# Kernel tuning notes

Measured on AMD Instinct MI355X. Metric: run time of the kernel, lower is better.

The kernel has to match this reference:

```python
import jax, jax.numpy as jnp
import numpy as np

B, N, C, H, R = 8, 1024, 768, 12, 64
HD = C // H


def setup_inputs() -> dict:
    key = jax.random.key(0)
    ks = jax.random.split(key, 16)
    def nrm(k, shape, s=0.02):
        return jax.random.normal(k, shape, jnp.float32) * s
    return {
        'x': jax.random.normal(ks[0], (B, N, C), jnp.float32),
        'Wqkv': nrm(ks[1], (3 * C, C)),
        'ssf_scale1': 1.0 + nrm(ks[2], (3 * C,)),
        'ssf_shift1': nrm(ks[3], (3 * C,)),
        'Wa': nrm(ks[4], (R, C)),            # LoRA down (sliced to sample_LoRA_dim)
        'Wb': nrm(ks[5], (3 * C, R)),        # LoRA up
        'Wrouter': nrm(ks[6], (2 * H * 3, C)),
        'brouter': nrm(ks[7], (2 * H * 3,)),
        'Wad_down': nrm(ks[8], (R, C)),      # parallel adapter down
        'bad_down': nrm(ks[9], (R,)),
        'Wad_up': nrm(ks[10], (3 * C, R)),   # parallel adapter up -> 3*dim
        'bad_up': nrm(ks[11], (3 * C,)),
        'Wproj': nrm(ks[12], (C, C)),
        'bproj': nrm(ks[13], (C,)),
        'ssf_scale2': 1.0 + nrm(ks[14], (C,)),
        'ssf_shift2': nrm(ks[15], (C,)),
    }


def reference(x, Wqkv, ssf_scale1, ssf_shift1, Wa, Wb, Wrouter, brouter,
              Wad_down, bad_down, Wad_up, bad_up, Wproj, bproj,
              ssf_scale2, ssf_shift2):
    Bx, Nx, Cx = x.shape
    scale = (Cx // H) ** -0.5

    def split_qkv(t):
        t = t.reshape(Bx, Nx, 3, H, Cx // H).transpose(2, 0, 3, 1, 4)
        return t[0], t[1], t[2]

    # base QKV with SSF scale-shift
    q, k, v = split_qkv((x @ Wqkv.T) * ssf_scale1 + ssf_shift1)
    # LoRA delta (dropout inactive at eval)
    ql, kl, vl = split_qkv((x @ Wa.T) @ Wb.T)
    # parallel adapter delta
    qp, kp, vp = split_qkv(jax.nn.gelu(x @ Wad_down.T + bad_down, approximate=False) @ Wad_up.T + bad_up)
    # router gating: sigmoid logits -> [B,N,3,H,2]
    rs = jax.nn.sigmoid(x @ Wrouter.T + brouter).reshape(Bx, Nx, 3, H, 2)
    # faithful to source: raw reshape [B,N,3,H] -> [B,N,H,3] (index-mixing), then transpose(1,2)
    rl = rs[..., 0].reshape(Bx, Nx, H, 3).transpose(0, 2, 1, 3)  # [B,H,N,3]
    rp = rs[..., 1].reshape(Bx, Nx, H, 3).transpose(0, 2, 1, 3)
    q = q + ql * rl[..., 0:1]
    k = k + kl * rl[..., 1:2] + kp * rp[..., 1:2]
    v = v + vl * rl[..., 2:3] + vp * rp[..., 2:3]
    # standard attention (prefix path disabled: prefix_dim=0)
    attn = jax.nn.softmax(jnp.einsum('bhnd,bhmd->bhnm', q, k) * scale, axis=-1)
    o = jnp.einsum('bhnm,bhmd->bhnd', attn, v).transpose(0, 2, 1, 3).reshape(Bx, Nx, Cx)
    return (o @ Wproj.T + bproj) * ssf_scale2 + ssf_shift2
```

## Files before the change

### kernel.cpp

```cpp
#include <hip/hip_runtime.h>
#include <math.h>

typedef unsigned short u16;
typedef unsigned int u32;
typedef short s16x8 __attribute__((ext_vector_type(8)));
typedef float f32x4 __attribute__((ext_vector_type(4)));
typedef float f32x16 __attribute__((ext_vector_type(16)));
typedef u16 u16x4 __attribute__((ext_vector_type(4)));

#define DEVI __device__ __forceinline__

DEVI u16 f2bf(float f) {
  unsigned u = __builtin_bit_cast(unsigned, f);
  u += 0x7fffu + ((u >> 16) & 1u);
  return (u16)(u >> 16);
}

DEVI u32 pkbf_hu(float a, float b) {
  const u32 ua = __builtin_bit_cast(u32, a) + 0x8000u;
  const u32 ub = __builtin_bit_cast(u32, b) + 0x8000u;
  return __builtin_amdgcn_perm(ub, ua, 0x07060302u);
}

DEVI f32x4 zero4() { f32x4 z; z[0]=0.f; z[1]=0.f; z[2]=0.f; z[3]=0.f; return z; }

DEVI float xor32_max(float x) { return fmaxf(x, __shfl_xor(x, 32, 64)); }
DEVI float xor32_sum(float x) { return x + __shfl_xor(x, 32, 64); }

#define MFMA16(a,b,c) __builtin_amdgcn_mfma_f32_16x16x32_bf16((a),(b),(c),0,0,0)
#define MFMA32(a,b,c) __builtin_amdgcn_mfma_f32_32x32x16_bf16((a),(b),(c),0,0,0)

#define GLD16(gp, lp) __builtin_amdgcn_global_load_lds( \
  (const __attribute__((address_space(1))) void*)(const void*)(gp), \
  (__attribute__((address_space(3))) void*)(void*)(lp), 16, 0, 0)

#define WAITVM(N) asm volatile("s_waitcnt vmcnt(" #N ")" ::: "memory")
#define WAITLG0() asm volatile("s_waitcnt lgkmcnt(0)" ::: "memory")
#define SBAR() __builtin_amdgcn_s_barrier()


__global__ __launch_bounds__(256) void prep_x(const float* __restrict__ x,
                                              u16* __restrict__ Aaug) {
  const int i = blockIdx.x * 256 + threadIdx.x;
  if (i >= 8192 * 192) return;
  const int row = i / 192, c4 = (i - row * 192) * 4;
  const float4 v = *(const float4*)(x + (size_t)row * 768 + c4);
  u16x4 o; o[0]=f2bf(v.x); o[1]=f2bf(v.y); o[2]=f2bf(v.z); o[3]=f2bf(v.w);
  *(u16x4*)(Aaug + (size_t)row * 896 + c4) = o;
}

__global__ __launch_bounds__(256) void prep_w(
    const float* __restrict__ Wqkv, const float* __restrict__ s1,
    const float* __restrict__ Wb, const float* __restrict__ Wup,
    const float* __restrict__ Wa, const float* __restrict__ Wdn,
    const float* __restrict__ Wr, const float* __restrict__ Wp,
    u16* __restrict__ Baug, u16* __restrict__ Wsm, u16* __restrict__ Wpj) {
  const int i = blockIdx.x * 256 + threadIdx.x;
  const int N1 = 2304 * 896, N2 = N1 + 256 * 768, N3 = N2 + 768 * 768;
  if (i < N1) {
    const int c = i / 896, kk = i - c * 896;
    float v;
    if (kk < 768)      v = Wqkv[(size_t)c * 768 + kk] * s1[c];
    else if (kk < 832) v = Wb[(size_t)c * 64 + (kk - 768)];
    else               v = Wup[(size_t)c * 64 + (kk - 832)];
    Baug[i] = f2bf(v);
  } else if (i < N2) {
    const int j = i - N1; const int r = j / 768, kk = j - r * 768;
    float v = 0.0f;
    if (r < 64)       v = Wa[(size_t)r * 768 + kk];
    else if (r < 128) v = Wdn[(size_t)(r - 64) * 768 + kk];
    else if (r < 200) v = Wr[(size_t)(r - 128) * 768 + kk];
    Wsm[j] = f2bf(v);
  } else if (i < N3) {
    const int j = i - N2;
    Wpj[j] = f2bf(Wp[j]);
  }
}


template <int MODE>
__global__ __launch_bounds__(256)
void gemm_mfma(const u16* __restrict__ A, int lda,
               const u16* __restrict__ Bt, int ldb,
               const float* __restrict__ p0, const float* __restrict__ p1,
               const float* __restrict__ p2,
               u16* __restrict__ ob0, u16* __restrict__ ob1, u16* __restrict__ ob2,
               float* __restrict__ of0,
               const float* __restrict__ gates) {
  __shared__ __align__(16) u16 lds[3][8192];
  __shared__ float glds[2][2][128];
  const int tid = threadIdx.x;
  const int w = tid >> 6, l = tid & 63;
  const int rl = l & 15, gq = l >> 4;
  const int wrow = (w >> 1) * 64, wcol = (w & 1) * 64;
  const int br = blockIdx.x, bc = blockIdx.y;
  const int nt = (MODE == 2) ? 28 : 24;

  const int srow = l >> 2;
  const int sslot = (l & 3) ^ ((srow >> 1) & 3);
  const u16* aSrc = A + (size_t)(br * 128 + w * 32 + srow) * lda + sslot * 8;
  const u16* bSrc = Bt + (size_t)(bc * 128 + w * 32 + srow) * ldb + sslot * 8;

  int tq = 0;
  if constexpr (MODE == 2) {
    const int g = bc * 2 + (w & 1);
    tq = g / 12;
  }

  auto kt_of = [&](int t) {
    if constexpr (MODE == 2) return (t < 2) ? 26 + t : ((t < 4) ? 22 + t : t - 4);
    else return t;
  };
  auto stage = [&](int kt, int buf) {
    const size_t k0 = (size_t)kt * 32;
    GLD16(aSrc + k0, &lds[buf][(w * 32) * 32]);
    GLD16(aSrc + k0 + (size_t)16 * lda, &lds[buf][(w * 32 + 16) * 32]);
    GLD16(bSrc + k0, &lds[buf][4096 + (w * 32) * 32]);
    GLD16(bSrc + k0 + (size_t)16 * ldb, &lds[buf][4096 + (w * 32 + 16) * 32]);
  };

  stage(kt_of(0), 0);
  stage(kt_of(1), 1);
  if constexpr (MODE == 2) {
    const int gsel = tid >> 7, rr = tid & 127;
    const int gg = bc * 2 + gsel;
    const int tt = gg / 12, hh = gg % 12;
    const int f = hh * 3 + tt;
    const int ridx = (f / 12) * 24 + (f % 12) * 2;
    glds[gsel][0][rr] = gates[(size_t)(br * 128 + rr) * 72 + ridx];
    glds[gsel][1][rr] = gates[(size_t)(br * 128 + rr) * 72 + ridx + 1];
    WAITLG0();
  }

  f32x4 acc[4][4];
#pragma unroll
  for (int i = 0; i < 4; ++i)
#pragma unroll
    for (int j = 0; j < 4; ++j) acc[i][j] = zero4();

  for (int t = 0; t < nt; ++t) {
    const int buf = t % 3;
    if (t + 2 < nt) stage(kt_of(t + 2), (t + 2) % 3);
    if (t < nt - 2)       WAITVM(8);
    else if (t == nt - 2) WAITVM(4);
    else                  WAITVM(0);
    SBAR();

    const int sl = gq ^ ((rl >> 1) & 3);
    s16x8 af[4], bfv[4];
#pragma unroll
    for (int fr = 0; fr < 4; ++fr) {
      const int row = wrow + fr * 16 + rl;
      af[fr] = *(const s16x8*)&lds[buf][row * 32 + sl * 8];
    }
#pragma unroll
    for (int fc = 0; fc < 4; ++fc) {
      const int row = wcol + fc * 16 + rl;
      bfv[fc] = *(const s16x8*)&lds[buf][4096 + row * 32 + sl * 8];
    }
#pragma unroll
    for (int fr = 0; fr < 4; ++fr)
#pragma unroll
      for (int fc = 0; fc < 4; ++fc)
        acc[fr][fc] = MFMA16(af[fr], bfv[fc], acc[fr][fc]);

    if constexpr (MODE == 2) {
      if (t == 1 || t == 3) {
        const int wsel = w & 1;
        const bool ad = (t == 1);
#pragma unroll
        for (int fr = 0; fr < 4; ++fr)
#pragma unroll
          for (int r = 0; r < 4; ++r) {
            const int rloc = wrow + fr * 16 + gq * 4 + r;
            const float gl = glds[wsel][0][rloc];
            float s;
            if (ad) { const float gp = glds[wsel][1][rloc]; s = (tq > 0) ? gp / gl : 0.0f; }
            else s = gl;
#pragma unroll
            for (int fc = 0; fc < 4; ++fc) acc[fr][fc][r] *= s;
          }
      }
    }
    SBAR();
  }

  if constexpr (MODE == 0) {
#pragma unroll
    for (int fc = 0; fc < 4; ++fc) {
      const int col = bc * 128 + wcol + fc * 16 + rl;
#pragma unroll
      for (int fr = 0; fr < 4; ++fr)
#pragma unroll
        for (int r = 0; r < 4; ++r) {
          const int grow = br * 128 + wrow + fr * 16 + gq * 4 + r;
          const float v = acc[fr][fc][r];
          if (col < 64) {
            ob0[(size_t)grow * 896 + 768 + col] = f2bf(v);
          } else if (col < 128) {
            const float u = v + p0[col - 64];
            const float gv = 0.5f * u * (1.0f + erff(u * 0.70710678118654752f));
            ob0[(size_t)grow * 896 + 832 + (col - 64)] = f2bf(gv);
          } else if (col < 200) {
            const float z = v + p1[col - 128];
            of0[(size_t)grow * 72 + (col - 128)] = 1.0f / (1.0f + expf(-z));
          }
        }
    }
  } else if constexpr (MODE == 1) {
#pragma unroll
    for (int fc = 0; fc < 4; ++fc) {
      const int col = bc * 128 + wcol + fc * 16 + rl;
      const float bb = p0[col], sc = p1[col], sf = p2[col];
#pragma unroll
      for (int fr = 0; fr < 4; ++fr)
#pragma unroll
        for (int r = 0; r < 4; ++r) {
          const int grow = br * 128 + wrow + fr * 16 + gq * 4 + r;
          of0[(size_t)grow * 768 + col] = (acc[fr][fc][r] + bb) * sc + sf;
        }
    }
  } else {
    const int wsel = w & 1;
    const int bq = br >> 3;
    const int n0 = (br & 7) * 128;
    const int cbase = bc * 128 + wcol;
    const int hh = (cbase % 768) / 64;
    float s1v[4], buv[4];
#pragma unroll
    for (int fc = 0; fc < 4; ++fc) {
      const int col = cbase + fc * 16 + rl;
      s1v[fc] = p0[col];
      buv[fc] = (tq > 0) ? p1[col] : 0.0f;
    }
    if (tq < 2) {
      u16* L = (u16*)&lds[0][0] + (size_t)w * 4096;
      u16* dst = (tq == 0) ? ob0 : ob1;
      const float osc = (tq == 0) ? 0.125f : 1.0f;
#pragma unroll
      for (int fr = 0; fr < 4; ++fr)
#pragma unroll
        for (int r = 0; r < 4; ++r) {
          const int nloc = fr * 16 + gq * 4 + r;
          const float gp = glds[wsel][1][wrow + nloc];
#pragma unroll
          for (int fc = 0; fc < 4; ++fc) {
            const int d = fc * 16 + rl;
            const float v = (acc[fr][fc][r] + s1v[fc] + gp * buv[fc]) * osc;
            L[nloc * 64 + (d ^ (gq << 4))] = f2bf(v);
          }
        }
      const size_t rowbase = (size_t)(bq * 12 + hh) * 1024 + n0 + wrow;
#pragma unroll
      for (int it = 0; it < 8; ++it) {
        const int nloc = it * 8 + (l >> 3);
        const int sl8 = l & 7;
        const s16x8 val =
            *(const s16x8*)&L[nloc * 64 + ((sl8 * 8) ^ (((nloc >> 2) & 3) << 4))];
        *(s16x8*)(dst + (rowbase + nloc) * 64 + sl8 * 8) = val;
      }
    } else {
      u16* L = (u16*)&lds[0][0] + (size_t)w * 4096;
#pragma unroll
      for (int fr = 0; fr < 4; ++fr)
#pragma unroll
        for (int r = 0; r < 4; ++r) {
          const int rloc = wrow + fr * 16 + gq * 4 + r;
          const float gp = glds[wsel][1][rloc];
          const int nloc = fr * 16 + gq * 4 + r;
#pragma unroll
          for (int fc = 0; fc < 4; ++fc) {
            const int d = fc * 16 + rl;
            const float v = acc[fr][fc][r] + s1v[fc] + gp * buv[fc];
            L[(d * 64 + nloc) ^ ((d & 7) << 3)] = f2bf(v);
          }
        }
      const int nw = n0 + wrow;
#pragma unroll
      for (int it = 0; it < 8; ++it) {
        const int d = it * 8 + (l >> 3);
        const int slot = l & 7;
        const s16x8 val = *(const s16x8*)&L[d * 64 + ((slot ^ (d & 7)) << 3)];
        *(s16x8*)(ob2 + ((size_t)(bq * 12 + hh) * 64 + d) * 1024 + nw + slot * 8) = val;
      }
    }
  }
}


__global__ __launch_bounds__(256)
void attn2_kernel(const u16* __restrict__ Q, const u16* __restrict__ K,
                  const u16* __restrict__ VT, u16* __restrict__ AO) {
  __shared__ __align__(16) u16 kv[3][8192];
  const int tid = threadIdx.x, w = tid >> 6, l = tid & 63;
  const int l31 = l & 31, hi = l >> 5;
  const int bh = blockIdx.x % 96, qt = blockIdx.x / 96;
  const size_t kb = (size_t)bh * (1024 * 64);
  const float LOG2E = 1.4426950408889634f;
  const float THR = 5.545177f;

  const int q0 = qt * 128 + w * 32;
  s16x8 qf[4];
  {
    const u16* qp = Q + kb + (size_t)(q0 + l31) * 64 + hi * 8;
#pragma unroll
    for (int ks = 0; ks < 4; ++ks) qf[ks] = *(const s16x8*)(qp + ks * 16);
  }

  const int srow = l >> 3;
  const int sslot = (l & 7) ^ srow;
  const u16* kSrc = K + kb + (size_t)(w * 16 + srow) * 64 + sslot * 8;
  const u16* vSrc = VT + kb + (size_t)(w * 16 + srow) * 1024 + sslot * 8;
  auto stage = [&](int t, int buf) {
    const int kv0 = t * 64;
    GLD16(kSrc + (size_t)kv0 * 64, &kv[buf][(w * 16) * 64]);
    GLD16(kSrc + (size_t)kv0 * 64 + 8 * 64, &kv[buf][(w * 16 + 8) * 64]);
    GLD16(vSrc + kv0, &kv[buf][4096 + (w * 16) * 64]);
    GLD16(vSrc + kv0 + 8 * 1024, &kv[buf][4096 + (w * 16 + 8) * 64]);
  };

  f32x16 o0, o1;
#pragma unroll
  for (int r = 0; r < 16; ++r) { o0[r] = 0.f; o1[r] = 0.f; }
  float m = -1.0e30f, lsum = 0.f;

  const int swz = l31 & 7;

  stage(0, 0);
  stage(1, 1);

  for (int t = 0; t < 16; ++t) {
    const int buf = t % 3;
    if (t + 2 < 16) stage(t + 2, (t + 2) % 3);
    if (t < 14)       WAITVM(8);
    else if (t == 14) WAITVM(4);
    else              WAITVM(0);
    SBAR();

    f32x16 sA, sB;
#pragma unroll
    for (int r = 0; r < 16; ++r) { sA[r] = 0.f; sB[r] = 0.f; }
#pragma unroll
    for (int ks = 0; ks < 4; ++ks) {
      const int slot = (ks * 2 + hi) ^ swz;
      const s16x8 k0 = *(const s16x8*)&kv[buf][l31 * 64 + slot * 8];
      const s16x8 k1 = *(const s16x8*)&kv[buf][(32 + l31) * 64 + slot * 8];
      sA = MFMA32(k0, qf[ks], sA);
      sB = MFMA32(k1, qf[ks], sB);
    }

    float pm = sA[0];
#pragma unroll
    for (int r = 1; r < 16; ++r) pm = fmaxf(pm, sA[r]);
#pragma unroll
    for (int r = 0; r < 16; ++r) pm = fmaxf(pm, sB[r]);
    pm = xor32_max(pm);

    const bool need = pm > m + THR;
    if (__any(need)) {
      const float mnew = need ? pm : m;
      const float corr = __builtin_amdgcn_exp2f((m - mnew) * LOG2E);
      m = mnew;
      lsum *= corr;
#pragma unroll
      for (int r = 0; r < 16; ++r) {
        const int qrow = (r & 3) + 8 * (r >> 2) + 4 * hi;
        const float cr = __shfl(corr, qrow, 64);
        o0[r] *= cr; o1[r] *= cr;
      }
    }

    const float mL = m * LOG2E;
    float ps = 0.f;
#pragma unroll
    for (int r = 0; r < 16; ++r) {
      const float p = __builtin_amdgcn_exp2f(__builtin_fmaf(sA[r], LOG2E, -mL));
      sA[r] = p; ps += p;
    }
#pragma unroll
    for (int r = 0; r < 16; ++r) {
      const float p = __builtin_amdgcn_exp2f(__builtin_fmaf(sB[r], LOG2E, -mL));
      sB[r] = p; ps += p;
    }
    lsum += xor32_sum(ps);

    s16x8 pf[4];
#pragma unroll
    for (int s = 0; s < 4; ++s) {
      const f32x16 P = (s < 2) ? sA : sB;
      const int b = 8 * (s & 1);
      const u32 A0 = pkbf_hu(P[b + 0], P[b + 1]);
      const u32 A1 = pkbf_hu(P[b + 2], P[b + 3]);
      const u32 A2 = pkbf_hu(P[b + 4], P[b + 5]);
      const u32 A3 = pkbf_hu(P[b + 6], P[b + 7]);
      const u32 B0 = (u32)__shfl_xor((int)A0, 32, 64);
      const u32 B1 = (u32)__shfl_xor((int)A1, 32, 64);
      const u32 B2 = (u32)__shfl_xor((int)A2, 32, 64);
      const u32 B3 = (u32)__shfl_xor((int)A3, 32, 64);
      union { u32 u[4]; s16x8 v; } pk;
      pk.u[0] = hi ? B2 : A0;
      pk.u[1] = hi ? B3 : A1;
      pk.u[2] = hi ? A2 : B0;
      pk.u[3] = hi ? A3 : B1;
      pf[s] = pk.v;
    }

#pragma unroll
    for (int s = 0; s < 4; ++s) {
      const int slot = (s * 2 + hi) ^ swz;
      const s16x8 v0 = *(const s16x8*)&kv[buf][4096 + l31 * 64 + slot * 8];
      const s16x8 v1 = *(const s16x8*)&kv[buf][4096 + (32 + l31) * 64 + slot * 8];
      o0 = MFMA32(pf[s], v0, o0);
      o1 = MFMA32(pf[s], v1, o1);
    }
    SBAR();
  }

  const float invl = 1.0f / lsum;
  const int bq = bh / 12, h = bh % 12;
#pragma unroll
  for (int r = 0; r < 16; ++r) {
    const int qrow = (r & 3) + 8 * (r >> 2) + 4 * hi;
    const float ir = __shfl(invl, qrow, 64);
    const int n = q0 + qrow;
    u16* dst = AO + ((size_t)bq * 1024 + n) * 768 + h * 64 + l31;
    dst[0]  = f2bf(o0[r] * ir);
    dst[32] = f2bf(o1[r] * ir);
  }
}


extern "C" void kernel_launch(void* const* d_in, const int* in_sizes, int n_in,
                              void* d_out, int out_size, void* d_ws, size_t ws_size,
                              hipStream_t stream) {
  (void)in_sizes; (void)n_in; (void)out_size; (void)ws_size;
  const float* x    = (const float*)d_in[0];
  const float* Wqkv = (const float*)d_in[1];
  const float* s1   = (const float*)d_in[2];
  const float* sh1  = (const float*)d_in[3];
  const float* Wa   = (const float*)d_in[4];
  const float* Wb   = (const float*)d_in[5];
  const float* Wr   = (const float*)d_in[6];
  const float* brt  = (const float*)d_in[7];
  const float* Wdn  = (const float*)d_in[8];
  const float* bdn  = (const float*)d_in[9];
  const float* Wup  = (const float*)d_in[10];
  const float* bup  = (const float*)d_in[11];
  const float* Wp   = (const float*)d_in[12];
  const float* bpj  = (const float*)d_in[13];
  const float* sc2  = (const float*)d_in[14];
  const float* sf2  = (const float*)d_in[15];
  float* out = (float*)d_out;

  char* ws = (char*)d_ws;
  size_t off = 0;
  auto take = [&](size_t bytes) -> void* {
    void* p = ws + off;
    off = (off + bytes + 255) & ~(size_t)255;
    return p;
  };
  u16* Aaug = (u16*)take(8192UL * 896 * 2);
  u16* Baug = (u16*)take(2304UL * 896 * 2);
  u16* Wsm  = (u16*)take(256UL * 768 * 2);
  u16* Wpj  = (u16*)take(768UL * 768 * 2);
  float* gates = (float*)take(8192UL * 72 * 4);
  u16* qb  = (u16*)take(96UL * 1024 * 64 * 2);
  u16* kbf = (u16*)take(96UL * 1024 * 64 * 2);
  u16* vtb = (u16*)take(96UL * 64 * 1024 * 2);
  u16* ao  = (u16*)take(8192UL * 768 * 2);

  prep_x<<<dim3(6144), dim3(256), 0, stream>>>(x, Aaug);
  prep_w<<<dim3(11136), dim3(256), 0, stream>>>(Wqkv, s1, Wb, Wup, Wa, Wdn, Wr, Wp,
                                                Baug, Wsm, Wpj);
  gemm_mfma<0><<<dim3(64, 2), dim3(256), 0, stream>>>(
      Aaug, 896, Wsm, 768, bdn, brt, nullptr, Aaug, nullptr, nullptr, gates, nullptr);
  gemm_mfma<2><<<dim3(64, 18), dim3(256), 0, stream>>>(
      Aaug, 896, Baug, 896, sh1, bup, nullptr, qb, kbf, vtb, nullptr, gates);
  attn2_kernel<<<dim3(768), dim3(256), 0, stream>>>(qb, kbf, vtb, ao);
  gemm_mfma<1><<<dim3(64, 6), dim3(256), 0, stream>>>(
      ao, 768, Wpj, 768, bpj, sc2, sf2, nullptr, nullptr, nullptr, out, nullptr);
}
```

Baseline: 174.2 us.

## Enlarge QKV GEMM tile to 256 rows with 512-thread blocks

The main QKV GEMM (MODE 2) now uses 256x128 tiles computed by 8 waves instead of 128x128 by 4 waves, which halves the grid along M. Each wave now stages one B row chunk instead of two, so each B tile is loaded once for twice as many A rows and global/LDS traffic for B drops. The vmcnt waits, gate LDS buffer and epilogue row indexing are adjusted to match. In exchange LDS use per block grows, the grid has fewer blocks (576), and the epilogue, which reuses lds per wave, has to remain correct with 8 waves.

Measured after the change: 179.8 us. 3.2% more time.

```diff
diff --git a/kernel.cpp b/kernel.cpp
--- a/kernel.cpp
+++ b/kernel.cpp
@@ -79,7 +79,7 @@
 
 
 template <int MODE>
-__global__ __launch_bounds__(256)
+__global__ __launch_bounds__((MODE == 2) ? 512 : 256)
 void gemm_mfma(const u16* __restrict__ A, int lda,
                const u16* __restrict__ Bt, int ldb,
                const float* __restrict__ p0, const float* __restrict__ p1,
@@ -87,19 +87,24 @@
                u16* __restrict__ ob0, u16* __restrict__ ob1, u16* __restrict__ ob2,
                float* __restrict__ of0,
                const float* __restrict__ gates) {
-  __shared__ __align__(16) u16 lds[3][8192];
-  __shared__ float glds[2][2][128];
+  constexpr int BM   = (MODE == 2) ? 256 : 128;
+  constexpr int BUFU = (MODE == 2) ? 12288 : 8192;
+  constexpr int BOFF = (MODE == 2) ? 8192 : 4096;
+  constexpr int nt   = (MODE == 2) ? 28 : 24;
+
+  __shared__ __align__(16) u16 lds[3][BUFU];
+  __shared__ float glds[2][2][BM];
   const int tid = threadIdx.x;
   const int w = tid >> 6, l = tid & 63;
   const int rl = l & 15, gq = l >> 4;
   const int wrow = (w >> 1) * 64, wcol = (w & 1) * 64;
   const int br = blockIdx.x, bc = blockIdx.y;
-  const int nt = (MODE == 2) ? 28 : 24;
 
   const int srow = l >> 2;
   const int sslot = (l & 3) ^ ((srow >> 1) & 3);
-  const u16* aSrc = A + (size_t)(br * 128 + w * 32 + srow) * lda + sslot * 8;
-  const u16* bSrc = Bt + (size_t)(bc * 128 + w * 32 + srow) * ldb + sslot * 8;
+  const u16* aSrc = A + (size_t)(br * BM + w * 32 + srow) * lda + sslot * 8;
+  const int bwrow = (MODE == 2) ? w * 16 : w * 32;
+  const u16* bSrc = Bt + (size_t)(bc * 128 + bwrow + srow) * ldb + sslot * 8;
 
   int tq = 0;
   if constexpr (MODE == 2) {
@@ -115,20 +120,24 @@
     const size_t k0 = (size_t)kt * 32;
     GLD16(aSrc + k0, &lds[buf][(w * 32) * 32]);
     GLD16(aSrc + k0 + (size_t)16 * lda, &lds[buf][(w * 32 + 16) * 32]);
-    GLD16(bSrc + k0, &lds[buf][4096 + (w * 32) * 32]);
-    GLD16(bSrc + k0 + (size_t)16 * ldb, &lds[buf][4096 + (w * 32 + 16) * 32]);
+    if constexpr (MODE == 2) {
+      GLD16(bSrc + k0, &lds[buf][BOFF + (w * 16) * 32]);
+    } else {
+      GLD16(bSrc + k0, &lds[buf][BOFF + (w * 32) * 32]);
+      GLD16(bSrc + k0 + (size_t)16 * ldb, &lds[buf][BOFF + (w * 32 + 16) * 32]);
+    }
   };
 
   stage(kt_of(0), 0);
   stage(kt_of(1), 1);
   if constexpr (MODE == 2) {
-    const int gsel = tid >> 7, rr = tid & 127;
+    const int gsel = tid >> 8, rr = tid & 255;
     const int gg = bc * 2 + gsel;
     const int tt = gg / 12, hh = gg % 12;
     const int f = hh * 3 + tt;
     const int ridx = (f / 12) * 24 + (f % 12) * 2;
-    glds[gsel][0][rr] = gates[(size_t)(br * 128 + rr) * 72 + ridx];
-    glds[gsel][1][rr] = gates[(size_t)(br * 128 + rr) * 72 + ridx + 1];
+    glds[gsel][0][rr] = gates[(size_t)(br * BM + rr) * 72 + ridx];
+    glds[gsel][1][rr] = gates[(size_t)(br * BM + rr) * 72 + ridx + 1];
     WAITLG0();
   }
 
@@ -141,9 +150,15 @@
   for (int t = 0; t < nt; ++t) {
     const int buf = t % 3;
     if (t + 2 < nt) stage(kt_of(t + 2), (t + 2) % 3);
-    if (t < nt - 2)       WAITVM(8);
-    else if (t == nt - 2) WAITVM(4);
-    else                  WAITVM(0);
+    if constexpr (MODE == 2) {
+      if (t < nt - 2)       WAITVM(6);
+      else if (t == nt - 2) WAITVM(3);
+      else                  WAITVM(0);
+    } else {
+      if (t < nt - 2)       WAITVM(8);
+      else if (t == nt - 2) WAITVM(4);
+      else                  WAITVM(0);
+    }
     SBAR();
 
     const int sl = gq ^ ((rl >> 1) & 3);
@@ -156,7 +171,7 @@
 #pragma unroll
     for (int fc = 0; fc < 4; ++fc) {
       const int row = wcol + fc * 16 + rl;
-      bfv[fc] = *(const s16x8*)&lds[buf][4096 + row * 32 + sl * 8];
+      bfv[fc] = *(const s16x8*)&lds[buf][BOFF + row * 32 + sl * 8];
     }
 #pragma unroll
     for (int fr = 0; fr < 4; ++fr)
@@ -222,8 +237,8 @@
     }
   } else {
     const int wsel = w & 1;
-    const int bq = br >> 3;
-    const int n0 = (br & 7) * 128;
+    const int bq = br >> 2;
+    const int n0 = (br & 3) * 256;
     const int cbase = bc * 128 + wcol;
     const int hh = (cbase % 768) / 64;
     float s1v[4], buv[4];
@@ -474,7 +489,7 @@
                                                 Baug, Wsm, Wpj);
   gemm_mfma<0><<<dim3(64, 2), dim3(256), 0, stream>>>(
       Aaug, 896, Wsm, 768, bdn, brt, nullptr, Aaug, nullptr, nullptr, gates, nullptr);
-  gemm_mfma<2><<<dim3(64, 18), dim3(256), 0, stream>>>(
+  gemm_mfma<2><<<dim3(32, 18), dim3(512), 0, stream>>>(
       Aaug, 896, Baug, 896, sh1, bup, nullptr, qb, kbf, vtb, nullptr, gates);
   attn2_kernel<<<dim3(768), dim3(256), 0, stream>>>(qb, kbf, vtb, ao);
   gemm_mfma<1><<<dim3(64, 6), dim3(256), 0, stream>>>(
```
